# Optimization experiments

Measured on AMD Instinct MI355X. Metric: run time of the kernel, lower is better.

Reference implementation:

```python
import jax, jax.numpy as jnp
import numpy as np


def _apply_rope(x, rope):
    # x: (B, T, D); rope: (T, D//2, 2) broadcast over batch
    B, T, D = x.shape
    x_ = x.reshape(B, T, D // 2, 2)
    cos, sin = rope[..., 0], rope[..., 1]
    xr, xi = x_[..., 0], x_[..., 1]
    rotr = xr * cos - xi * sin
    roti = xr * sin + xi * cos
    return jnp.stack([rotr, roti], axis=-1).reshape(B, T, D)


def setup_inputs() -> dict:
    key = jax.random.key(0)
    k1, k2, k3, k4 = jax.random.split(key, 4)
    B, T, D, H = 2, 2048, 1024, 16
    x = jax.random.normal(k1, (B, T, D), dtype=jnp.float32)
    rope = jax.random.normal(k2, (T, D // 2, 2), dtype=jnp.float32)
    w_qkv = jax.random.normal(k3, (3 * D, D), dtype=jnp.float32) * (1.0 / np.sqrt(D))
    w_proj = jax.random.normal(k4, (D, D), dtype=jnp.float32) * (1.0 / np.sqrt(D))
    return {"x": x, "rope": rope, "w_qkv": w_qkv, "w_proj": w_proj}


def reference(x, rope, w_qkv, w_proj):
    B, T, D = x.shape
    H = 16
    dk = D // H
    qkv = jnp.einsum("btd,ed->bte", x, w_qkv)  # (B, T, 3D)
    q, k, v = jnp.split(qkv, 3, axis=-1)
    q = _apply_rope(q, rope)
    k = _apply_rope(k, rope)
    # split heads: (B, H, T, dk)
    q = q.reshape(B, T, H, dk).transpose(0, 2, 1, 3)
    k = k.reshape(B, T, H, dk).transpose(0, 2, 1, 3)
    v = v.reshape(B, T, H, dk).transpose(0, 2, 1, 3)
    att = jnp.einsum("bhqd,bhkd->bhqk", q, k) / jnp.sqrt(jnp.float32(dk)).astype(x.dtype)
    att = jax.nn.softmax(att, axis=-1)
    out = jnp.einsum("bhqk,bhkd->bhqd", att, v)
    out = out.transpose(0, 2, 1, 3).reshape(B, T, D)
    return jnp.einsum("btd,ed->bte", out, w_proj)
```

## Files before the change

### kernel.cpp

```cpp
#include <hip/hip_runtime.h>

typedef _Float16 f16;
typedef _Float16 f16x2 __attribute__((ext_vector_type(2)));
typedef _Float16 f16x4 __attribute__((ext_vector_type(4)));
typedef _Float16 f16x8 __attribute__((ext_vector_type(8)));
typedef float    f32x2 __attribute__((ext_vector_type(2)));
typedef float    f32x4 __attribute__((ext_vector_type(4)));

#define GLDS16(gptr, lptr)                                                     \
  __builtin_amdgcn_global_load_lds(                                            \
      (const __attribute__((address_space(1))) void*)(gptr),                   \
      (__attribute__((address_space(3))) void*)(lptr), 16, 0, 0)

__global__ __launch_bounds__(256) void k_cast(const float* __restrict__ in,
                                              f16* __restrict__ out, int n4) {
  int i = blockIdx.x * 256 + threadIdx.x;
  if (i >= n4) return;
  f32x4 v = ((const f32x4*)in)[i];
  f16x4 h;
  h[0] = (f16)v[0]; h[1] = (f16)v[1]; h[2] = (f16)v[2]; h[3] = (f16)v[3];
  ((f16x4*)out)[i] = h;
}

__global__ __launch_bounds__(256, 4) void k_gemm_bt(const f16* __restrict__ A,
                                                    const f16* __restrict__ B,
                                                    void* __restrict__ Cout,
                                                    int M, int N, int K,
                                                    int out_is_f16) {
  __shared__ f16 sA[128 * 64];
  __shared__ f16 sB[128 * 64];
  const int tid = threadIdx.x;
  const int wave = tid >> 6, lane = tid & 63;
  const int lr = lane & 15, lq = lane >> 4;
  const int lr7 = lr & 7;
  const int wm = (wave >> 1) * 64, wn = (wave & 1) * 64;
  const size_t m0 = (size_t)blockIdx.x * 128, n0 = (size_t)blockIdx.y * 128;

  f32x4 acc[4][4] = {};

  const int sw8 = ((tid & 7) ^ ((tid >> 3) & 7)) * 8;
  const f16* ga = A + (m0 + (tid >> 3)) * (size_t)K + sw8;
  const f16* gb = B + (n0 + (tid >> 3)) * (size_t)K + sw8;

  for (int k0 = 0; k0 < K; k0 += 64) {
    __syncthreads();
#pragma unroll
    for (int r = 0; r < 4; ++r) {
      GLDS16(ga + (size_t)(r * 32) * K + k0, (char*)sA + r * 4096 + wave * 1024);
      GLDS16(gb + (size_t)(r * 32) * K + k0, (char*)sB + r * 4096 + wave * 1024);
    }
    __syncthreads();

#pragma unroll
    for (int kk = 0; kk < 2; ++kk) {
      f16x8 af[4], bf[4];
#pragma unroll
      for (int i = 0; i < 4; ++i)
        af[i] = *(const f16x8*)&sA[(wm + i * 16 + lr) * 64 +
                                   (((kk * 4 + lq) ^ lr7) * 8)];
#pragma unroll
      for (int j = 0; j < 4; ++j)
        bf[j] = *(const f16x8*)&sB[(wn + j * 16 + lr) * 64 +
                                   (((kk * 4 + lq) ^ lr7) * 8)];
#pragma unroll
      for (int i = 0; i < 4; ++i)
#pragma unroll
        for (int j = 0; j < 4; ++j)
          acc[i][j] = __builtin_amdgcn_mfma_f32_16x16x32_f16(af[i], bf[j],
                                                             acc[i][j], 0, 0, 0);
    }
  }

  if (out_is_f16) {
    f16* C = (f16*)Cout;
#pragma unroll
    for (int i = 0; i < 4; ++i)
#pragma unroll
      for (int j = 0; j < 4; ++j)
#pragma unroll
        for (int r = 0; r < 4; ++r)
          C[(m0 + wm + i * 16 + lq * 4 + r) * (size_t)N + n0 + wn + j * 16 + lr] =
              (f16)acc[i][j][r];
  } else {
    float* C = (float*)Cout;
#pragma unroll
    for (int i = 0; i < 4; ++i)
#pragma unroll
      for (int j = 0; j < 4; ++j)
#pragma unroll
        for (int r = 0; r < 4; ++r)
          C[(m0 + wm + i * 16 + lq * 4 + r) * (size_t)N + n0 + wn + j * 16 + lr] =
              acc[i][j][r];
  }
}

__global__ __launch_bounds__(256) void k_rope(const f16* __restrict__ qkv,
                                              const float* __restrict__ rope,
                                              f16* __restrict__ qh,
                                              f16* __restrict__ kh) {
  int idx = blockIdx.x * 256 + threadIdx.x;
  int pair = idx & 1023, t = (idx >> 10) & 2047, b = idx >> 21;
  int which = pair >> 9, p = pair & 511;
  const f16* src = qkv + ((size_t)(b * 2048 + t)) * 3072 + which * 1024 + p * 2;
  f16x2 s2 = *(const f16x2*)src;
  float xr = (float)s2[0], xi = (float)s2[1];
  f32x2 cs = *(const f32x2*)(rope + ((size_t)t * 512 + p) * 2);
  float scl = which ? 1.0f : 0.125f * 1.44269504088896f;
  float rr = (xr * cs[0] - xi * cs[1]) * scl;
  float ri = (xr * cs[1] + xi * cs[0]) * scl;
  int h = p >> 5, cc = (p & 31) * 2;
  f16* dst = (which ? kh : qh) + ((size_t)(b * 16 + h) * 2048 + t) * 64 + cc;
  f16x2 o; o[0] = (f16)rr; o[1] = (f16)ri;
  *(f16x2*)dst = o;
}

__global__ __launch_bounds__(256) void k_transpv(const f16* __restrict__ qkv,
                                                 f16* __restrict__ vt) {
  int bh = blockIdx.x >> 5, tt = blockIdx.x & 31;
  int b = bh >> 4, h = bh & 15;
  __shared__ f16 tile[64][65];
  int tid = threadIdx.x;
  int r = tid >> 4, c4 = (tid & 15) * 4;
#pragma unroll
  for (int rr = 0; rr < 4; ++rr) {
    int row = rr * 16 + r;
    const f16* src =
        qkv + ((size_t)(b * 2048 + tt * 64 + row)) * 3072 + 2048 + h * 64 + c4;
    f16x4 v = *(const f16x4*)src;
    tile[row][c4 + 0] = v[0]; tile[row][c4 + 1] = v[1];
    tile[row][c4 + 2] = v[2]; tile[row][c4 + 3] = v[3];
  }
  __syncthreads();
#pragma unroll
  for (int rr = 0; rr < 4; ++rr) {
    int c = rr * 16 + r;
    int t4 = (tid & 15) * 4;
    f16x4 o;
    o[0] = tile[t4 + 0][c]; o[1] = tile[t4 + 1][c];
    o[2] = tile[t4 + 2][c]; o[3] = tile[t4 + 3][c];
    *(f16x4*)(vt + ((size_t)(bh * 64 + c)) * 2048 + tt * 64 + t4) = o;
  }
}

__global__ __launch_bounds__(256, 3) void k_attn(const f16* __restrict__ Qp,
                                                 const f16* __restrict__ Kp,
                                                 const f16* __restrict__ Vt,
                                                 f16* __restrict__ Op) {
  __shared__ f16 sQ[128 * 64];
  __shared__ f16 sK[128 * 64];
  __shared__ f16 sV[64 * 128];
  const int tid = threadIdx.x, wave = tid >> 6, lane = tid & 63;
  const int lr = lane & 15, lq = lane >> 4;
  const int lr7 = lr & 7;
  const int bh = blockIdx.x, qt = blockIdx.y;
  const size_t base = (size_t)bh * 2048 * 64;

  const int sw8 = ((tid & 7) ^ ((tid >> 3) & 7)) * 8;
  const int sw16 = ((tid & 15) ^ ((tid >> 4) & 15)) * 8;

  const f16* gq = Qp + base + (size_t)qt * 128 * 64;
#pragma unroll
  for (int r = 0; r < 4; ++r)
    GLDS16(gq + (size_t)(r * 32 + (tid >> 3)) * 64 + sw8,
           (char*)sQ + r * 4096 + wave * 1024);
  __syncthreads();
  f16x8 qa0 = *(const f16x8*)&sQ[(wave * 32 + lr) * 64 + ((lq ^ lr7) * 8)];
  f16x8 qa1 = *(const f16x8*)&sQ[(wave * 32 + lr) * 64 + (((4 + lq) ^ lr7) * 8)];
  f16x8 qb0 = *(const f16x8*)&sQ[(wave * 32 + 16 + lr) * 64 + ((lq ^ lr7) * 8)];
  f16x8 qb1 =
      *(const f16x8*)&sQ[(wave * 32 + 16 + lr) * 64 + (((4 + lq) ^ lr7) * 8)];

  f32x4 ota[4] = {}, otb[4] = {};
  float ma = -__builtin_inff(), mb = -__builtin_inff();
  float la = 0.f, lb = 0.f;

  for (int jc = 0; jc < 16; ++jc) {
    __syncthreads();
    const f16* gk = Kp + base + (size_t)jc * 128 * 64;
    const f16* gv = Vt + base + (size_t)jc * 128;
#pragma unroll
    for (int r = 0; r < 4; ++r) {
      GLDS16(gk + (size_t)(r * 32 + (tid >> 3)) * 64 + sw8,
             (char*)sK + r * 4096 + wave * 1024);
      GLDS16(gv + (size_t)(r * 16 + (tid >> 4)) * 2048 + sw16,
             (char*)sV + r * 4096 + wave * 1024);
    }
    __syncthreads();

    f32x4 sta[8], stb[8];
#pragma unroll
    for (int nt = 0; nt < 8; ++nt) {
      f16x8 kf0 = *(const f16x8*)&sK[(nt * 16 + lr) * 64 + ((lq ^ lr7) * 8)];
      f16x8 kf1 =
          *(const f16x8*)&sK[(nt * 16 + lr) * 64 + (((4 + lq) ^ lr7) * 8)];
      f32x4 z = {0.f, 0.f, 0.f, 0.f};
      f32x4 sa = __builtin_amdgcn_mfma_f32_16x16x32_f16(kf0, qa0, z, 0, 0, 0);
      sta[nt] = __builtin_amdgcn_mfma_f32_16x16x32_f16(kf1, qa1, sa, 0, 0, 0);
      f32x4 sb = __builtin_amdgcn_mfma_f32_16x16x32_f16(kf0, qb0, z, 0, 0, 0);
      stb[nt] = __builtin_amdgcn_mfma_f32_16x16x32_f16(kf1, qb1, sb, 0, 0, 0);
    }

    float mla = -__builtin_inff(), mlb = -__builtin_inff();
#pragma unroll
    for (int nt = 0; nt < 8; ++nt)
#pragma unroll
      for (int r = 0; r < 4; ++r) {
        mla = fmaxf(mla, sta[nt][r]);
        mlb = fmaxf(mlb, stb[nt][r]);
      }
    mla = fmaxf(mla, __shfl_xor(mla, 16));
    mla = fmaxf(mla, __shfl_xor(mla, 32));
    mlb = fmaxf(mlb, __shfl_xor(mlb, 16));
    mlb = fmaxf(mlb, __shfl_xor(mlb, 32));
    float mna = fmaxf(ma, mla), mnb = fmaxf(mb, mlb);
    float aa = __builtin_amdgcn_exp2f(ma - mna);
    float ab = __builtin_amdgcn_exp2f(mb - mnb);
    ma = mna; mb = mnb;
    la *= aa; lb *= ab;

    f16x4 pfa[8], pfb[8];
#pragma unroll
    for (int nt = 0; nt < 8; ++nt) {
#pragma unroll
      for (int r = 0; r < 4; ++r) {
        float pa = __builtin_amdgcn_exp2f(sta[nt][r] - mna);
        float pb = __builtin_amdgcn_exp2f(stb[nt][r] - mnb);
        la += pa; lb += pb;
        pfa[nt][r] = (f16)pa; pfb[nt][r] = (f16)pb;
      }
    }
#pragma unroll
    for (int d = 0; d < 4; ++d) { ota[d] *= aa; otb[d] *= ab; }

#pragma unroll
    for (int d = 0; d < 4; ++d)
#pragma unroll
      for (int ks = 0; ks < 8; ++ks) {
        int vslot = (ks * 2 + (lq >> 1)) ^ lr;
        f16x4 vf = *(const f16x4*)&sV[(d * 16 + lr) * 128 + vslot * 8 +
                                      (lq & 1) * 4];
        ota[d] = __builtin_amdgcn_mfma_f32_16x16x16f16(vf, pfa[ks], ota[d],
                                                       0, 0, 0);
        otb[d] = __builtin_amdgcn_mfma_f32_16x16x16f16(vf, pfb[ks], otb[d],
                                                       0, 0, 0);
      }
  }

  la += __shfl_xor(la, 16); la += __shfl_xor(la, 32);
  lb += __shfl_xor(lb, 16); lb += __shfl_xor(lb, 32);
  float rla = 1.f / la, rlb = 1.f / lb;
  int b = bh >> 4, h = bh & 15;
  int ta = qt * 128 + wave * 32 + lr;
  f16* gouta = Op + ((size_t)(b * 2048 + ta)) * 1024 + h * 64;
  f16* goutb = gouta + (size_t)16 * 1024;
#pragma unroll
  for (int d = 0; d < 4; ++d) {
    f16x4 oa, ob;
#pragma unroll
    for (int r = 0; r < 4; ++r) {
      oa[r] = (f16)(ota[d][r] * rla);
      ob[r] = (f16)(otb[d][r] * rlb);
    }
    *(f16x4*)&gouta[d * 16 + lq * 4] = oa;
    *(f16x4*)&goutb[d * 16 + lq * 4] = ob;
  }
}

extern "C" void kernel_launch(void* const* d_in, const int* in_sizes, int n_in,
                              void* d_out, int out_size, void* d_ws,
                              size_t ws_size, hipStream_t stream) {
  const float* x     = (const float*)d_in[0];
  const float* rope  = (const float*)d_in[1];
  const float* wqkv  = (const float*)d_in[2];
  const float* wproj = (const float*)d_in[3];
  float* out = (float*)d_out;

  char* w = (char*)d_ws;
  const size_t MB = 1024 * 1024;
  f16* xh   = (f16*)(w + 0);
  f16* qh   = (f16*)(w + 0);
  f16* wqh  = (f16*)(w + 8 * MB);
  f16* wph  = (f16*)(w + 14 * MB);
  f16* qkvh = (f16*)(w + 16 * MB);
  f16* aoh  = (f16*)(w + 16 * MB);
  f16* kh   = (f16*)(w + 40 * MB);
  f16* vth  = (f16*)(w + 48 * MB);

  k_cast<<<4096, 256, 0, stream>>>(x, xh, 1048576);
  k_cast<<<3072, 256, 0, stream>>>(wqkv, wqh, 786432);
  k_cast<<<1024, 256, 0, stream>>>(wproj, wph, 262144);

  k_gemm_bt<<<dim3(32, 24), 256, 0, stream>>>(xh, wqh, (void*)qkvh, 4096, 3072,
                                              1024, 1);
  k_rope<<<16384, 256, 0, stream>>>(qkvh, rope, qh, kh);
  k_transpv<<<1024, 256, 0, stream>>>(qkvh, vth);

  k_attn<<<dim3(32, 16), 256, 0, stream>>>(qh, kh, vth, aoh);

  k_gemm_bt<<<dim3(32, 8), 256, 0, stream>>>(aoh, wph, (void*)out, 4096, 1024,
                                             1024, 0);
}
```

Measured before the change: 202.6 us.

## Fuse RoPE and V transpose into QKV GEMM epilogue, double-buffer attention K/V

Merges the three cast launches into one kernel. Moves the RoPE rotation and scaling of Q/K, plus the V transpose, into the QKV GEMM epilogue, which removes the intermediate qkv buffer round trip and two kernel launches. Double-buffers the K/V shared-memory tiles in attention using explicit vmcnt waits so the next tile loads while the current one computes. The larger LDS footprint lowers the occupancy hint from 3 to 2 blocks, and the fused epilogue does scattered 2-byte stores with per-element rope loads.

```diff
diff --git a/kernel.cpp b/kernel.cpp
--- a/kernel.cpp
+++ b/kernel.cpp
@@ -12,21 +12,36 @@
       (const __attribute__((address_space(1))) void*)(gptr),                   \
       (__attribute__((address_space(3))) void*)(lptr), 16, 0, 0)
 
-__global__ __launch_bounds__(256) void k_cast(const float* __restrict__ in,
-                                              f16* __restrict__ out, int n4) {
+#define S_BARRIER() __builtin_amdgcn_s_barrier()
+#define FENCE() asm volatile("" ::: "memory")
+#define WAIT_VM8() asm volatile("s_waitcnt vmcnt(8)" ::: "memory")
+#define WAIT_VM0() asm volatile("s_waitcnt vmcnt(0)" ::: "memory")
+#define WAIT_LGKM0() asm volatile("s_waitcnt lgkmcnt(0)" ::: "memory")
+
+__global__ __launch_bounds__(256) void k_cast3(const float* __restrict__ a,
+                                               const float* __restrict__ b,
+                                               const float* __restrict__ c,
+                                               f16* __restrict__ oa,
+                                               f16* __restrict__ ob,
+                                               f16* __restrict__ oc) {
   int i = blockIdx.x * 256 + threadIdx.x;
-  if (i >= n4) return;
-  f32x4 v = ((const f32x4*)in)[i];
+  const float* src;
+  f16* dst;
+  int off;
+  if (i < 1048576) { src = a; dst = oa; off = i; }
+  else if (i < 1835008) { src = b; dst = ob; off = i - 1048576; }
+  else { src = c; dst = oc; off = i - 1835008; }
+  f32x4 v = ((const f32x4*)src)[off];
   f16x4 h;
   h[0] = (f16)v[0]; h[1] = (f16)v[1]; h[2] = (f16)v[2]; h[3] = (f16)v[3];
-  ((f16x4*)out)[i] = h;
-}
-
-__global__ __launch_bounds__(256, 4) void k_gemm_bt(const f16* __restrict__ A,
-                                                    const f16* __restrict__ B,
-                                                    void* __restrict__ Cout,
-                                                    int M, int N, int K,
-                                                    int out_is_f16) {
+  ((f16x4*)dst)[off] = h;
+}
+
+__global__ __launch_bounds__(256, 4) void k_gemm_qkv(
+    const f16* __restrict__ A, const f16* __restrict__ B,
+    const float* __restrict__ rope, f16* __restrict__ qh,
+    f16* __restrict__ kh, f16* __restrict__ vt) {
+  const int K = 1024;
   __shared__ f16 sA[128 * 64];
   __shared__ f16 sB[128 * 64];
   const int tid = threadIdx.x;
@@ -71,84 +86,111 @@
     }
   }
 
-  if (out_is_f16) {
-    f16* C = (f16*)Cout;
+  const int region = (int)(n0 >> 10);
+  if (region == 2) {
 #pragma unroll
     for (int i = 0; i < 4; ++i)
 #pragma unroll
+      for (int j = 0; j < 4; ++j) {
+        int e = (int)(n0 + wn + j * 16 + lr) - 2048;
+        int h = e >> 6, c = e & 63;
+        int m = (int)(m0 + wm + i * 16 + lq * 4);
+        int b = m >> 11, t0 = m & 2047;
+        f16x4 o;
+#pragma unroll
+        for (int r = 0; r < 4; ++r) o[r] = (f16)acc[i][j][r];
+        *(f16x4*)&vt[(((size_t)(b * 16 + h)) * 64 + c) * 2048 + t0] = o;
+      }
+  } else {
+    const float scl = region == 0 ? 0.1803368801111204f : 1.0f;
+    f16* dst = region == 0 ? qh : kh;
+    const int odd = lr & 1;
+#pragma unroll
+    for (int i = 0; i < 4; ++i)
+#pragma unroll
+      for (int j = 0; j < 4; ++j) {
+        int e = ((int)(n0 + wn + j * 16 + lr)) & 1023;
+        int h = e >> 6, c = e & 63, p = e >> 1;
+        int mb = (int)(m0 + wm + i * 16 + lq * 4);
+        int b = mb >> 11;
+#pragma unroll
+        for (int r = 0; r < 4; ++r) {
+          int t = (mb + r) & 2047;
+          float v = acc[i][j][r];
+          float partner = __shfl_xor(v, 1);
+          f32x2 cs = *(const f32x2*)&rope[((size_t)t * 512 + p) * 2];
+          float out = odd ? (partner * cs[1] + v * cs[0])
+                          : (v * cs[0] - partner * cs[1]);
+          dst[(((size_t)(b * 16 + h)) * 2048 + t) * 64 + c] = (f16)(out * scl);
+        }
+      }
+  }
+}
+
+__global__ __launch_bounds__(256, 4) void k_gemm_bt(const f16* __restrict__ A,
+                                                    const f16* __restrict__ B,
+                                                    float* __restrict__ C,
+                                                    int M, int N, int K) {
+  __shared__ f16 sA[128 * 64];
+  __shared__ f16 sB[128 * 64];
+  const int tid = threadIdx.x;
+  const int wave = tid >> 6, lane = tid & 63;
+  const int lr = lane & 15, lq = lane >> 4;
+  const int lr7 = lr & 7;
+  const int wm = (wave >> 1) * 64, wn = (wave & 1) * 64;
+  const size_t m0 = (size_t)blockIdx.x * 128, n0 = (size_t)blockIdx.y * 128;
+
+  f32x4 acc[4][4] = {};
+
+  const int sw8 = ((tid & 7) ^ ((tid >> 3) & 7)) * 8;
+  const f16* ga = A + (m0 + (tid >> 3)) * (size_t)K + sw8;
+  const f16* gb = B + (n0 + (tid >> 3)) * (size_t)K + sw8;
+
+  for (int k0 = 0; k0 < K; k0 += 64) {
+    __syncthreads();
+#pragma unroll
+    for (int r = 0; r < 4; ++r) {
+      GLDS16(ga + (size_t)(r * 32) * K + k0, (char*)sA + r * 4096 + wave * 1024);
+      GLDS16(gb + (size_t)(r * 32) * K + k0, (char*)sB + r * 4096 + wave * 1024);
+    }
+    __syncthreads();
+
+#pragma unroll
+    for (int kk = 0; kk < 2; ++kk) {
+      f16x8 af[4], bf[4];
+#pragma unroll
+      for (int i = 0; i < 4; ++i)
+        af[i] = *(const f16x8*)&sA[(wm + i * 16 + lr) * 64 +
+                                   (((kk * 4 + lq) ^ lr7) * 8)];
+#pragma unroll
       for (int j = 0; j < 4; ++j)
-#pragma unroll
-        for (int r = 0; r < 4; ++r)
-          C[(m0 + wm + i * 16 + lq * 4 + r) * (size_t)N + n0 + wn + j * 16 + lr] =
-              (f16)acc[i][j][r];
-  } else {
-    float* C = (float*)Cout;
-#pragma unroll
-    for (int i = 0; i < 4; ++i)
-#pragma unroll
-      for (int j = 0; j < 4; ++j)
-#pragma unroll
-        for (int r = 0; r < 4; ++r)
-          C[(m0 + wm + i * 16 + lq * 4 + r) * (size_t)N + n0 + wn + j * 16 + lr] =
-              acc[i][j][r];
-  }
-}
-
-__global__ __launch_bounds__(256) void k_rope(const f16* __restrict__ qkv,
-                                              const float* __restrict__ rope,
-                                              f16* __restrict__ qh,
-                                              f16* __restrict__ kh) {
-  int idx = blockIdx.x * 256 + threadIdx.x;
-  int pair = idx & 1023, t = (idx >> 10) & 2047, b = idx >> 21;
-  int which = pair >> 9, p = pair & 511;
-  const f16* src = qkv + ((size_t)(b * 2048 + t)) * 3072 + which * 1024 + p * 2;
-  f16x2 s2 = *(const f16x2*)src;
-  float xr = (float)s2[0], xi = (float)s2[1];
-  f32x2 cs = *(const f32x2*)(rope + ((size_t)t * 512 + p) * 2);
-  float scl = which ? 1.0f : 0.125f * 1.44269504088896f;
-  float rr = (xr * cs[0] - xi * cs[1]) * scl;
-  float ri = (xr * cs[1] + xi * cs[0]) * scl;
-  int h = p >> 5, cc = (p & 31) * 2;
-  f16* dst = (which ? kh : qh) + ((size_t)(b * 16 + h) * 2048 + t) * 64 + cc;
-  f16x2 o; o[0] = (f16)rr; o[1] = (f16)ri;
-  *(f16x2*)dst = o;
-}
-
-__global__ __launch_bounds__(256) void k_transpv(const f16* __restrict__ qkv,
-                                                 f16* __restrict__ vt) {
-  int bh = blockIdx.x >> 5, tt = blockIdx.x & 31;
-  int b = bh >> 4, h = bh & 15;
-  __shared__ f16 tile[64][65];
-  int tid = threadIdx.x;
-  int r = tid >> 4, c4 = (tid & 15) * 4;
-#pragma unroll
-  for (int rr = 0; rr < 4; ++rr) {
-    int row = rr * 16 + r;
-    const f16* src =
-        qkv + ((size_t)(b * 2048 + tt * 64 + row)) * 3072 + 2048 + h * 64 + c4;
-    f16x4 v = *(const f16x4*)src;
-    tile[row][c4 + 0] = v[0]; tile[row][c4 + 1] = v[1];
-    tile[row][c4 + 2] = v[2]; tile[row][c4 + 3] = v[3];
-  }
-  __syncthreads();
-#pragma unroll
-  for (int rr = 0; rr < 4; ++rr) {
-    int c = rr * 16 + r;
-    int t4 = (tid & 15) * 4;
-    f16x4 o;
-    o[0] = tile[t4 + 0][c]; o[1] = tile[t4 + 1][c];
-    o[2] = tile[t4 + 2][c]; o[3] = tile[t4 + 3][c];
-    *(f16x4*)(vt + ((size_t)(bh * 64 + c)) * 2048 + tt * 64 + t4) = o;
-  }
-}
-
-__global__ __launch_bounds__(256, 3) void k_attn(const f16* __restrict__ Qp,
+        bf[j] = *(const f16x8*)&sB[(wn + j * 16 + lr) * 64 +
+                                   (((kk * 4 + lq) ^ lr7) * 8)];
+#pragma unroll
+      for (int i = 0; i < 4; ++i)
+#pragma unroll
+        for (int j = 0; j < 4; ++j)
+          acc[i][j] = __builtin_amdgcn_mfma_f32_16x16x32_f16(af[i], bf[j],
+                                                             acc[i][j], 0, 0, 0);
+    }
+  }
+
+#pragma unroll
+  for (int i = 0; i < 4; ++i)
+#pragma unroll
+    for (int j = 0; j < 4; ++j)
+#pragma unroll
+      for (int r = 0; r < 4; ++r)
+        C[(m0 + wm + i * 16 + lq * 4 + r) * (size_t)N + n0 + wn + j * 16 + lr] =
+            acc[i][j][r];
+}
+
+__global__ __launch_bounds__(256, 2) void k_attn(const f16* __restrict__ Qp,
                                                  const f16* __restrict__ Kp,
                                                  const f16* __restrict__ Vt,
                                                  f16* __restrict__ Op) {
   __shared__ f16 sQ[128 * 64];
-  __shared__ f16 sK[128 * 64];
-  __shared__ f16 sV[64 * 128];
+  __shared__ f16 sKV[2 * 16384];
   const int tid = threadIdx.x, wave = tid >> 6, lane = tid & 63;
   const int lr = lane & 15, lq = lane >> 4;
   const int lr7 = lr & 7;
@@ -158,12 +200,29 @@
   const int sw8 = ((tid & 7) ^ ((tid >> 3) & 7)) * 8;
   const int sw16 = ((tid & 15) ^ ((tid >> 4) & 15)) * 8;
 
+  auto stage_kv = [&](int jcc, int d) {
+    const f16* gk = Kp + base + (size_t)jcc * 128 * 64;
+    const f16* gv = Vt + base + (size_t)jcc * 128;
+    char* bK = (char*)sKV + d * 32768;
+    char* bV = bK + 16384;
+#pragma unroll
+    for (int r = 0; r < 4; ++r) {
+      GLDS16(gk + (size_t)(r * 32 + (tid >> 3)) * 64 + sw8,
+             bK + r * 4096 + wave * 1024);
+      GLDS16(gv + (size_t)(r * 16 + (tid >> 4)) * 2048 + sw16,
+             bV + r * 4096 + wave * 1024);
+    }
+  };
+
   const f16* gq = Qp + base + (size_t)qt * 128 * 64;
 #pragma unroll
   for (int r = 0; r < 4; ++r)
     GLDS16(gq + (size_t)(r * 32 + (tid >> 3)) * 64 + sw8,
            (char*)sQ + r * 4096 + wave * 1024);
-  __syncthreads();
+  stage_kv(0, 0);
+  WAIT_VM8();
+  S_BARRIER();
+  FENCE();
   f16x8 qa0 = *(const f16x8*)&sQ[(wave * 32 + lr) * 64 + ((lq ^ lr7) * 8)];
   f16x8 qa1 = *(const f16x8*)&sQ[(wave * 32 + lr) * 64 + (((4 + lq) ^ lr7) * 8)];
   f16x8 qb0 = *(const f16x8*)&sQ[(wave * 32 + 16 + lr) * 64 + ((lq ^ lr7) * 8)];
@@ -174,25 +233,27 @@
   float ma = -__builtin_inff(), mb = -__builtin_inff();
   float la = 0.f, lb = 0.f;
 
+#pragma unroll 1
   for (int jc = 0; jc < 16; ++jc) {
-    __syncthreads();
-    const f16* gk = Kp + base + (size_t)jc * 128 * 64;
-    const f16* gv = Vt + base + (size_t)jc * 128;
-#pragma unroll
-    for (int r = 0; r < 4; ++r) {
-      GLDS16(gk + (size_t)(r * 32 + (tid >> 3)) * 64 + sw8,
-             (char*)sK + r * 4096 + wave * 1024);
-      GLDS16(gv + (size_t)(r * 16 + (tid >> 4)) * 2048 + sw16,
-             (char*)sV + r * 4096 + wave * 1024);
-    }
-    __syncthreads();
+    const int cur = jc & 1;
+    if (jc < 15) {
+      stage_kv(jc + 1, cur ^ 1);
+      WAIT_VM8();
+    } else {
+      WAIT_VM0();
+    }
+    S_BARRIER();
+    FENCE();
+
+    const f16* bK = (const f16*)((char*)sKV + cur * 32768);
+    const f16* bV = bK + 8192;
 
     f32x4 sta[8], stb[8];
 #pragma unroll
     for (int nt = 0; nt < 8; ++nt) {
-      f16x8 kf0 = *(const f16x8*)&sK[(nt * 16 + lr) * 64 + ((lq ^ lr7) * 8)];
+      f16x8 kf0 = *(const f16x8*)&bK[(nt * 16 + lr) * 64 + ((lq ^ lr7) * 8)];
       f16x8 kf1 =
-          *(const f16x8*)&sK[(nt * 16 + lr) * 64 + (((4 + lq) ^ lr7) * 8)];
+          *(const f16x8*)&bK[(nt * 16 + lr) * 64 + (((4 + lq) ^ lr7) * 8)];
       f32x4 z = {0.f, 0.f, 0.f, 0.f};
       f32x4 sa = __builtin_amdgcn_mfma_f32_16x16x32_f16(kf0, qa0, z, 0, 0, 0);
       sta[nt] = __builtin_amdgcn_mfma_f32_16x16x32_f16(kf1, qa1, sa, 0, 0, 0);
@@ -237,13 +298,17 @@
 #pragma unroll
       for (int ks = 0; ks < 8; ++ks) {
         int vslot = (ks * 2 + (lq >> 1)) ^ lr;
-        f16x4 vf = *(const f16x4*)&sV[(d * 16 + lr) * 128 + vslot * 8 +
+        f16x4 vf = *(const f16x4*)&bV[(d * 16 + lr) * 128 + vslot * 8 +
                                       (lq & 1) * 4];
         ota[d] = __builtin_amdgcn_mfma_f32_16x16x16f16(vf, pfa[ks], ota[d],
                                                        0, 0, 0);
         otb[d] = __builtin_amdgcn_mfma_f32_16x16x16f16(vf, pfb[ks], otb[d],
                                                        0, 0, 0);
       }
+
+    WAIT_LGKM0();
+    S_BARRIER();
+    FENCE();
   }
 
   la += __shfl_xor(la, 16); la += __shfl_xor(la, 32);
@@ -277,26 +342,19 @@
 
   char* w = (char*)d_ws;
   const size_t MB = 1024 * 1024;
-  f16* xh   = (f16*)(w + 0);
-  f16* qh   = (f16*)(w + 0);
-  f16* wqh  = (f16*)(w + 8 * MB);
-  f16* wph  = (f16*)(w + 14 * MB);
-  f16* qkvh = (f16*)(w + 16 * MB);
-  f16* aoh  = (f16*)(w + 16 * MB);
-  f16* kh   = (f16*)(w + 40 * MB);
-  f16* vth  = (f16*)(w + 48 * MB);
-
-  k_cast<<<4096, 256, 0, stream>>>(x, xh, 1048576);
-  k_cast<<<3072, 256, 0, stream>>>(wqkv, wqh, 786432);
-  k_cast<<<1024, 256, 0, stream>>>(wproj, wph, 262144);
-
-  k_gemm_bt<<<dim3(32, 24), 256, 0, stream>>>(xh, wqh, (void*)qkvh, 4096, 3072,
-                                              1024, 1);
-  k_rope<<<16384, 256, 0, stream>>>(qkvh, rope, qh, kh);
-  k_transpv<<<1024, 256, 0, stream>>>(qkvh, vth);
+  f16* xh  = (f16*)(w + 0);
+  f16* wqh = (f16*)(w + 8 * MB);
+  f16* wph = (f16*)(w + 14 * MB);
+  f16* qh  = (f16*)(w + 16 * MB);
+  f16* kh  = (f16*)(w + 24 * MB);
+  f16* vth = (f16*)(w + 32 * MB);
+  f16* aoh = (f16*)(w + 40 * MB);
+
+  k_cast3<<<8192, 256, 0, stream>>>(x, wqkv, wproj, xh, wqh, wph);
+
+  k_gemm_qkv<<<dim3(32, 24), 256, 0, stream>>>(xh, wqh, rope, qh, kh, vth);
 
   k_attn<<<dim3(32, 16), 256, 0, stream>>>(qh, kh, vth, aoh);
 
-  k_gemm_bt<<<dim3(32, 8), 256, 0, stream>>>(aoh, wph, (void*)out, 4096, 1024,
-                                             1024, 0);
-}
+  k_gemm_bt<<<dim3(32, 8), 256, 0, stream>>>(aoh, wph, out, 4096, 1024, 1024);
+}
```

After: 186.5 us. 7.9% less time.
